# Performance work log

Measured on AMD Instinct MI355X. Metric: run time of the kernel, lower is better.

## Reference

```python
import jax, jax.numpy as jnp
import numpy as np

N = 50000
E = 800000
IN_C = 256
HID = 256
OUT_C = 64
HEADS = 4
NEG_SLOPE = 0.2  # PyG GATConv default leaky_relu slope


def gat_conv(x, edge_index, W, a_src, a_dst, bias, heads, concat):
    """PyG-style GATConv (add_self_loops=True, eval mode so no dropout).
    x: [N, F_in]; W: [F_in, heads*C]; a_src/a_dst: [heads, C]; bias: [heads*C] or [C].
    """
    n = x.shape[0]
    # add self loops
    loops = jnp.arange(n, dtype=edge_index.dtype)
    src = jnp.concatenate([edge_index[0], loops])
    dst = jnp.concatenate([edge_index[1], loops])
    h = (x @ W).reshape(n, heads, -1)               # [N, H, C]
    alpha_src = jnp.einsum('nhc,hc->nh', h, a_src)  # [N, H]
    alpha_dst = jnp.einsum('nhc,hc->nh', h, a_dst)
    e = jax.nn.leaky_relu(alpha_src[src] + alpha_dst[dst], NEG_SLOPE)  # [E', H]
    # segment softmax over incoming edges of each dst node
    m = jax.ops.segment_max(e, dst, num_segments=n)        # [N, H]
    w = jnp.exp(e - m[dst])
    denom = jax.ops.segment_sum(w, dst, num_segments=n)    # [N, H]
    att = w / (denom[dst] + 1e-16)                          # [E', H]
    out = jax.ops.segment_sum(h[src] * att[:, :, None], dst, num_segments=n)  # [N, H, C]
    out = out.reshape(n, -1) if concat else out.mean(axis=1)
    return out + bias


def setup_inputs() -> dict:
    key = jax.random.key(0)
    ks = jax.random.split(key, 10)
    c1 = HID // HEADS  # per-head channels of layer 1
    s_in = 1.0 / np.sqrt(IN_C)
    s_hid = 1.0 / np.sqrt(HID)
    return {
        'x': jax.random.normal(ks[0], (N, IN_C), dtype=jnp.float32),
        'edge_index': jax.random.randint(ks[1], (2, E), 0, N, dtype=jnp.int64),
        'W1': jax.random.normal(ks[2], (IN_C, HEADS * c1), dtype=jnp.float32) * s_in,
        'a_src1': jax.random.normal(ks[3], (HEADS, c1), dtype=jnp.float32) * s_in,
        'a_dst1': jax.random.normal(ks[4], (HEADS, c1), dtype=jnp.float32) * s_in,
        'b1': jnp.zeros((HEADS * c1,), dtype=jnp.float32),
        'W2': jax.random.normal(ks[5], (HID, OUT_C), dtype=jnp.float32) * s_hid,
        'a_src2': jax.random.normal(ks[6], (1, OUT_C), dtype=jnp.float32) * s_hid,
        'a_dst2': jax.random.normal(ks[7], (1, OUT_C), dtype=jnp.float32) * s_hid,
        'b2': jnp.zeros((OUT_C,), dtype=jnp.float32),
    }


def reference(x, edge_index, W1, a_src1, a_dst1, b1, W2, a_src2, a_dst2, b2):
    h = gat_conv(x, edge_index, W1, a_src1, a_dst1, b1, heads=HEADS, concat=True)
    h = jax.nn.elu(h)
    # dropout: eval mode -> identity
    return gat_conv(h, edge_index, W2, a_src2, a_dst2, b2, heads=1, concat=False)
```

## Files before the change

### kernel.cpp

```cpp
#include <hip/hip_runtime.h>
#include <math.h>

#define NN 50000
#define NE 800000
#define ET (NE + NN)
#define FIN 256
#define HIDC 256
#define OC 64
#define NH 4
#define NEG 0.2f
#define CAP 64
#define NSTRIPES (NN / 16)

typedef __attribute__((ext_vector_type(8))) short bf16x8;
typedef __attribute__((ext_vector_type(4))) float f32x4;

__device__ __forceinline__ unsigned short f2bf(float f) {
    unsigned u = __float_as_uint(f);
    unsigned r = (u + 0x7FFFu + ((u >> 16) & 1u)) >> 16;
    return (unsigned short)r;
}
__device__ __forceinline__ float bflo(unsigned v) { return __uint_as_float(v << 16); }
__device__ __forceinline__ float bfhi(unsigned v) { return __uint_as_float(v & 0xffff0000u); }

#define SCB 8
#define NB_SC ((ET + 256 * SCB - 1) / (256 * SCB))

__device__ __forceinline__ void scatter_body(const int* __restrict__ ei,
                                             int* __restrict__ cnt,
                                             unsigned short* __restrict__ esrc,
                                             int b, int tid) {
    int ebase = b * (256 * SCB) + tid;
    int s[SCB], d[SCB], k[SCB];
    bool v[SCB];
#pragma unroll
    for (int i = 0; i < SCB; i++) {
        int e = ebase + i * 256;
        v[i] = (e < ET);
        s[i] = 0; d[i] = 0;
        if (v[i]) {
            if (e < NE) { s[i] = ei[e]; d[i] = ei[NE + e]; }
            else { s[i] = d[i] = e - NE; }
        }
    }
#pragma unroll
    for (int i = 0; i < SCB; i++)
        if (v[i]) k[i] = atomicAdd(&cnt[d[i]], 1);
#pragma unroll
    for (int i = 0; i < SCB; i++)
        if (v[i] && k[i] < CAP) esrc[(size_t)d[i] * CAP + k[i]] = (unsigned short)s[i];
}

#define NB_CV (NN * FIN / 8 / 256)
#define NB_P1 32
#define NB_P2 8

__device__ __forceinline__ void pack_body(const float* __restrict__ W,
                                          unsigned short* __restrict__ Bp,
                                          int N, int NTL, int t) {
    int lane = t & 63;
    int ntl = (t >> 6) % NTL;
    int ks = ((t >> 6) / NTL) & 7;
    int hy = t / (64 * NTL * 8);
    int col = hy * NTL * 16 + ntl * 16 + (lane & 15);
    int k0 = ks * 32 + (lane >> 4) * 8;
#pragma unroll
    for (int i = 0; i < 8; i++) Bp[(size_t)t * 8 + i] = f2bf(W[(k0 + i) * N + col]);
}

__global__ void k_prep(const float* __restrict__ x, unsigned short* __restrict__ xb,
                       const float* __restrict__ W1, unsigned short* __restrict__ Bp1,
                       const float* __restrict__ W2, unsigned short* __restrict__ Bp2) {
    int b = blockIdx.x, tid = threadIdx.x;
    if (b < NB_CV) {
        int i = (b * 256 + tid) * 8;
        float4 f0 = *(const float4*)&x[i];
        float4 f1 = *(const float4*)&x[i + 4];
        uint4 o;
        o.x = (unsigned)f2bf(f0.x) | ((unsigned)f2bf(f0.y) << 16);
        o.y = (unsigned)f2bf(f0.z) | ((unsigned)f2bf(f0.w) << 16);
        o.z = (unsigned)f2bf(f1.x) | ((unsigned)f2bf(f1.y) << 16);
        o.w = (unsigned)f2bf(f1.z) | ((unsigned)f2bf(f1.w) << 16);
        *(uint4*)&xb[i] = o;
    } else if (b < NB_CV + NB_P1) {
        pack_body(W1, Bp1, HIDC, 8, (b - NB_CV) * 256 + tid);
    } else {
        pack_body(W2, Bp2, OC, 4, (b - NB_CV - NB_P1) * 256 + tid);
    }
}

template <int NTL, int NHEADS, bool SCAT>
__global__ void __launch_bounds__(256) k_gemm(const unsigned short* __restrict__ A,
                                              const unsigned short* __restrict__ Bp,
                                              unsigned short* __restrict__ D, int N,
                                              const float* __restrict__ aS,
                                              const float* __restrict__ aD,
                                              float* __restrict__ asOut,
                                              float* __restrict__ adOut,
                                              const int* __restrict__ ei,
                                              int* __restrict__ cnt,
                                              unsigned short* __restrict__ esrc) {
    constexpr int TOT = 8 * NTL * 64 * 8;
    constexpr int HPH = (NTL * 16) / 64;
    constexpr int CH = NTL * 16;
    __shared__ unsigned short sd[4][16][CH];
    if (SCAT && blockIdx.y == 0) {
        scatter_body(ei, cnt, esrc, blockIdx.x, threadIdx.x);
        return;
    }
    int yb = SCAT ? (int)blockIdx.y - 1 : (int)blockIdx.y;
    const unsigned short* bsrc = Bp + (size_t)yb * TOT;
    int wave = threadIdx.x >> 6, lane = threadIdx.x & 63;
    int l15 = lane & 15, lh = lane >> 4;
    int coloff = yb * CH;
    float aSv[NTL], aDv[NTL];
#pragma unroll
    for (int nt = 0; nt < NTL; nt++) {
        aSv[nt] = aS[coloff + nt * 16 + l15];
        aDv[nt] = aD[coloff + nt * 16 + l15];
    }
    for (int st = blockIdx.x * 4 + wave; st < NSTRIPES; st += gridDim.x * 4) {
        const unsigned short* arow = A + (size_t)(st * 16 + l15) * 256 + lh * 8;
        bf16x8 a[8];
#pragma unroll
        for (int ks = 0; ks < 8; ks++) a[ks] = *(const bf16x8*)(arow + ks * 32);
        f32x4 acc[NTL];
#pragma unroll
        for (int t = 0; t < NTL; t++) acc[t] = (f32x4){0.f, 0.f, 0.f, 0.f};
#pragma unroll
        for (int ks = 0; ks < 8; ks++) {
#pragma unroll
            for (int nt = 0; nt < NTL; nt++) {
                bf16x8 b = *(const bf16x8*)&bsrc[((size_t)(ks * NTL + nt) * 64 + lane) * 8];
                acc[nt] = __builtin_amdgcn_mfma_f32_16x16x32_bf16(a[ks], b, acc[nt], 0, 0, 0);
            }
        }
        int strow = st * 16;
#pragma unroll
        for (int nt = 0; nt < NTL; nt++)
#pragma unroll
            for (int r = 0; r < 4; r++)
                sd[wave][lh * 4 + r][nt * 16 + l15] = f2bf(acc[nt][r]);
        unsigned short* dbase = D + (size_t)strow * N + coloff;
        int row = lane >> 2, q = lane & 3;
#pragma unroll
        for (int it = 0; it < NTL / 2; it++) {
            int c8 = it * 4 + q;
            uint4 v = *(const uint4*)&sd[wave][row][c8 * 8];
            *(uint4*)&dbase[(size_t)row * N + c8 * 8] = v;
        }
#pragma unroll
        for (int r = 0; r < 4; r++) {
#pragma unroll
            for (int gg = 0; gg < HPH; gg++) {
                float ps = 0.f, pd = 0.f;
#pragma unroll
                for (int q2 = 0; q2 < 4; q2++) {
                    int nt = gg * 4 + q2;
                    ps += acc[nt][r] * aSv[nt];
                    pd += acc[nt][r] * aDv[nt];
                }
#pragma unroll
                for (int off = 1; off < 16; off <<= 1) {
                    ps += __shfl_xor(ps, off);
                    pd += __shfl_xor(pd, off);
                }
                if (l15 == 0) {
                    int rowi = strow + lh * 4 + r;
                    int hidx = yb * HPH + gg;
                    asOut[rowi * NHEADS + hidx] = ps;
                    adOut[rowi * NHEADS + hidx] = pd;
                }
            }
        }
    }
}

__global__ void k_agg1f(const int* __restrict__ cnt, const unsigned short* __restrict__ esrc,
                        const unsigned short* __restrict__ h, const float* __restrict__ as,
                        const float* __restrict__ ad, const float* __restrict__ bias,
                        unsigned short* __restrict__ out) {
    __shared__ float wlds[4][64][4];
    int wave = threadIdx.x >> 6;
    int n = blockIdx.x * 4 + wave;
    int lane = threadIdx.x & 63;
    if (n >= NN) return;
    int deg = cnt[n];
    deg = deg < CAP ? deg : CAP;
    const unsigned short* bucket = &esrc[(size_t)n * CAP];
    bool act = lane < deg;
    int myS = act ? (int)bucket[lane] : 0;
    float4 adv = *(const float4*)&ad[n * NH];
    float e0 = -INFINITY, e1 = -INFINITY, e2 = -INFINITY, e3 = -INFINITY;
    if (act) {
        float4 av = *(const float4*)&as[myS * NH];
        e0 = av.x + adv.x; e0 = e0 > 0.f ? e0 : NEG * e0;
        e1 = av.y + adv.y; e1 = e1 > 0.f ? e1 : NEG * e1;
        e2 = av.z + adv.z; e2 = e2 > 0.f ? e2 : NEG * e2;
        e3 = av.w + adv.w; e3 = e3 > 0.f ? e3 : NEG * e3;
    }
    float m0 = e0, m1 = e1, m2 = e2, m3 = e3;
    for (int off = 32; off; off >>= 1) {
        m0 = fmaxf(m0, __shfl_xor(m0, off));
        m1 = fmaxf(m1, __shfl_xor(m1, off));
        m2 = fmaxf(m2, __shfl_xor(m2, off));
        m3 = fmaxf(m3, __shfl_xor(m3, off));
    }
    float w0 = act ? expf(e0 - m0) : 0.f;
    float w1 = act ? expf(e1 - m1) : 0.f;
    float w2 = act ? expf(e2 - m2) : 0.f;
    float w3 = act ? expf(e3 - m3) : 0.f;
    *(float4*)&wlds[wave][lane][0] = (float4){w0, w1, w2, w3};
    float s0 = w0, s1 = w1, s2 = w2, s3 = w3;
    for (int off = 32; off; off >>= 1) {
        s0 += __shfl_xor(s0, off);
        s1 += __shfl_xor(s1, off);
        s2 += __shfl_xor(s2, off);
        s3 += __shfl_xor(s3, off);
    }
    int hh = lane >> 4;
    int cbase = hh * 64 + (lane & 15) * 4;
    float ssel = hh == 0 ? s0 : hh == 1 ? s1 : hh == 2 ? s2 : s3;
    float rsel = 1.f / (ssel + 1e-16f);
    const float* wcol = &wlds[wave][0][hh];
    const unsigned short* hb = h + cbase;
    float acc0 = 0.f, acc1 = 0.f, acc2 = 0.f, acc3 = 0.f;
    int degP = (deg + 7) & ~7;
    for (int j = 0; j < degP; j += 8) {
        uint2 pv[8];
        float wj[8];
#pragma unroll
        for (int u = 0; u < 8; u++) {
            int s = __shfl(myS, j + u);
            wj[u] = wcol[(j + u) * 4];
            pv[u] = *(const uint2*)&hb[(size_t)s * HIDC];
        }
#pragma unroll
        for (int u = 0; u < 8; u++) {
            acc0 += wj[u] * bflo(pv[u].x);
            acc1 += wj[u] * bfhi(pv[u].x);
            acc2 += wj[u] * bflo(pv[u].y);
            acc3 += wj[u] * bfhi(pv[u].y);
        }
    }
    float4 bv = *(const float4*)&bias[cbase];
    float v0 = acc0 * rsel + bv.x; v0 = v0 > 0.f ? v0 : expm1f(v0);
    float v1 = acc1 * rsel + bv.y; v1 = v1 > 0.f ? v1 : expm1f(v1);
    float v2 = acc2 * rsel + bv.z; v2 = v2 > 0.f ? v2 : expm1f(v2);
    float v3 = acc3 * rsel + bv.w; v3 = v3 > 0.f ? v3 : expm1f(v3);
    uint2 ov;
    ov.x = (unsigned)f2bf(v0) | ((unsigned)f2bf(v1) << 16);
    ov.y = (unsigned)f2bf(v2) | ((unsigned)f2bf(v3) << 16);
    *(uint2*)&out[(size_t)n * HIDC + cbase] = ov;
}

__global__ void k_agg2f(const int* __restrict__ cnt, const unsigned short* __restrict__ esrc,
                        const unsigned short* __restrict__ h, const float* __restrict__ as,
                        const float* __restrict__ ad, const float* __restrict__ bias,
                        float* __restrict__ out) {
    __shared__ float wlds[4][64];
    int wave = threadIdx.x >> 6;
    int n = blockIdx.x * 4 + wave;
    int lane = threadIdx.x & 63;
    if (n >= NN) return;
    int deg = cnt[n];
    deg = deg < CAP ? deg : CAP;
    const unsigned short* bucket = &esrc[(size_t)n * CAP];
    bool act = lane < deg;
    int myS = act ? (int)bucket[lane] : 0;
    float adv = ad[n];
    float e = -INFINITY;
    if (act) {
        e = as[myS] + adv;
        e = e > 0.f ? e : NEG * e;
    }
    float m = e;
    for (int off = 32; off; off >>= 1) m = fmaxf(m, __shfl_xor(m, off));
    float w = act ? expf(e - m) : 0.f;
    wlds[wave][lane] = w;
    float s = w;
    for (int off = 32; off; off >>= 1) s += __shfl_xor(s, off);
    float rd = 1.f / (s + 1e-16f);

    int sub = lane >> 4;
    int cw = (lane & 15) * 4;
    const unsigned short* hb = h + cw;
    float acc0 = 0.f, acc1 = 0.f, acc2 = 0.f, acc3 = 0.f;
    int degP = (deg + 7) & ~7;
    for (int j = 0; j < degP; j += 8) {
        uint2 pv[2];
        float wj[2];
#pragma unroll
        for (int u = 0; u < 2; u++) {
            int jj = j + u * 4 + sub;
            int sj = __shfl(myS, jj);
            wj[u] = wlds[wave][jj];
            pv[u] = *(const uint2*)&hb[(size_t)sj * OC];
        }
#pragma unroll
        for (int u = 0; u < 2; u++) {
            acc0 += wj[u] * bflo(pv[u].x);
            acc1 += wj[u] * bfhi(pv[u].x);
            acc2 += wj[u] * bflo(pv[u].y);
            acc3 += wj[u] * bfhi(pv[u].y);
        }
    }
#pragma unroll
    for (int off = 16; off < 64; off <<= 1) {
        acc0 += __shfl_xor(acc0, off);
        acc1 += __shfl_xor(acc1, off);
        acc2 += __shfl_xor(acc2, off);
        acc3 += __shfl_xor(acc3, off);
    }
    if (lane < 16) {
        float4 bv = *(const float4*)&bias[cw];
        float4 o;
        o.x = acc0 * rd + bv.x;
        o.y = acc1 * rd + bv.y;
        o.z = acc2 * rd + bv.z;
        o.w = acc3 * rd + bv.w;
        *(float4*)&out[(size_t)n * OC + cw] = o;
    }
}

extern "C" void kernel_launch(void* const* d_in, const int* in_sizes, int n_in,
                              void* d_out, int out_size, void* d_ws, size_t ws_size,
                              hipStream_t stream) {
    const float* x   = (const float*)d_in[0];
    const int*   ei  = (const int*)d_in[1];
    const float* W1  = (const float*)d_in[2];
    const float* aS1 = (const float*)d_in[3];
    const float* aD1 = (const float*)d_in[4];
    const float* b1  = (const float*)d_in[5];
    const float* W2  = (const float*)d_in[6];
    const float* aS2 = (const float*)d_in[7];
    const float* aD2 = (const float*)d_in[8];
    const float* b2  = (const float*)d_in[9];
    float* out = (float*)d_out;

    char* p = (char*)d_ws;
    auto alloc = [&](size_t nbytes) {
        char* r = p;
        p += (nbytes + 255) & ~(size_t)255;
        return r;
    };
    unsigned short* xb    = (unsigned short*)alloc((size_t)NN * FIN * 2);
    unsigned short* h1b   = (unsigned short*)alloc((size_t)NN * HIDC * 2);
    unsigned short* act1b = (unsigned short*)alloc((size_t)NN * HIDC * 2);
    unsigned short* h2b   = (unsigned short*)alloc((size_t)NN * OC * 2);
    unsigned short* Bp1   = (unsigned short*)alloc((size_t)2 * 8 * 8 * 64 * 8 * 2);
    unsigned short* Bp2   = (unsigned short*)alloc((size_t)1 * 8 * 4 * 64 * 8 * 2);
    float* as1  = (float*)alloc((size_t)NN * NH * 4);
    float* ad1  = (float*)alloc((size_t)NN * NH * 4);
    float* as2  = (float*)alloc((size_t)NN * 4);
    float* ad2  = (float*)alloc((size_t)NN * 4);
    int*   cnt  = (int*)alloc((size_t)NN * 4);
    unsigned short* esrc = (unsigned short*)alloc((size_t)NN * CAP * 2);

    hipMemsetAsync(cnt, 0, (size_t)NN * 4, stream);

    k_prep<<<NB_CV + NB_P1 + NB_P2, 256, 0, stream>>>(x, xb, W1, Bp1, W2, Bp2);

    k_gemm<8, NH, true><<<dim3(NB_SC, 3), 256, 0, stream>>>(xb, Bp1, h1b, HIDC,
                                                            aS1, aD1, as1, ad1,
                                                            ei, cnt, esrc);
    k_agg1f<<<(NN + 3) / 4, 256, 0, stream>>>(cnt, esrc, h1b, as1, ad1, b1, act1b);

    k_gemm<4, 1, false><<<dim3(391, 1), 256, 0, stream>>>(act1b, Bp2, h2b, OC,
                                                          aS2, aD2, as2, ad2,
                                                          nullptr, nullptr, nullptr);
    k_agg2f<<<(NN + 3) / 4, 256, 0, stream>>>(cnt, esrc, h2b, as2, ad2, b2, out);
}
```

Before: 194.5 us.

## Partition edge scatter by destination range and pad GEMM LDS staging rows

The edge-bucketing scatter now gives each block a fixed destination-node partition (one of 8) and a chunk of edges. Each block reads its whole chunk but only does atomics and stores for destinations in its partition, so concurrent atomics and esrc writes stay in a localized address range for better cache locality. The cost is that every edge is read 8 times. Separately, the shared-memory staging tile in the GEMM gets 8 padding elements per row to reduce LDS bank conflicts.

```diff
diff --git a/kernel.cpp b/kernel.cpp
--- a/kernel.cpp
+++ b/kernel.cpp
@@ -23,32 +23,30 @@
 __device__ __forceinline__ float bflo(unsigned v) { return __uint_as_float(v << 16); }
 __device__ __forceinline__ float bfhi(unsigned v) { return __uint_as_float(v & 0xffff0000u); }
 
-#define SCB 8
-#define NB_SC ((ET + 256 * SCB - 1) / (256 * SCB))
+#define NB_SC 416
+#define NPART 8
+#define PSZ (NN / NPART)
+#define NSUB (NB_SC / NPART)
 
 __device__ __forceinline__ void scatter_body(const int* __restrict__ ei,
                                              int* __restrict__ cnt,
                                              unsigned short* __restrict__ esrc,
                                              int b, int tid) {
-    int ebase = b * (256 * SCB) + tid;
-    int s[SCB], d[SCB], k[SCB];
-    bool v[SCB];
-#pragma unroll
-    for (int i = 0; i < SCB; i++) {
-        int e = ebase + i * 256;
-        v[i] = (e < ET);
-        s[i] = 0; d[i] = 0;
-        if (v[i]) {
-            if (e < NE) { s[i] = ei[e]; d[i] = ei[NE + e]; }
-            else { s[i] = d[i] = e - NE; }
-        }
-    }
-#pragma unroll
-    for (int i = 0; i < SCB; i++)
-        if (v[i]) k[i] = atomicAdd(&cnt[d[i]], 1);
-#pragma unroll
-    for (int i = 0; i < SCB; i++)
-        if (v[i] && k[i] < CAP) esrc[(size_t)d[i] * CAP + k[i]] = (unsigned short)s[i];
+    int p = b & (NPART - 1);
+    int q = b >> 3;
+    int lo = p * PSZ, hi = lo + PSZ;
+    const int chunk = (ET + NSUB - 1) / NSUB;
+    int e0 = q * chunk;
+    int e1 = e0 + chunk; if (e1 > ET) e1 = ET;
+    for (int e = e0 + tid; e < e1; e += 256) {
+        int s, d;
+        if (e < NE) { s = ei[e]; d = ei[NE + e]; }
+        else { s = d = e - NE; }
+        if (d >= lo && d < hi) {
+            int k = atomicAdd(&cnt[d], 1);
+            if (k < CAP) esrc[(size_t)d * CAP + k] = (unsigned short)s;
+        }
+    }
 }
 
 #define NB_CV (NN * FIN / 8 / 256)
@@ -103,7 +101,8 @@
     constexpr int TOT = 8 * NTL * 64 * 8;
     constexpr int HPH = (NTL * 16) / 64;
     constexpr int CH = NTL * 16;
-    __shared__ unsigned short sd[4][16][CH];
+    constexpr int CHP = CH + 8;
+    __shared__ unsigned short sd[4][16][CHP];
     if (SCAT && blockIdx.y == 0) {
         scatter_body(ei, cnt, esrc, blockIdx.x, threadIdx.x);
         return;
```

Result: slower. 242.7 us (+24.8%).
